# Kernel optimization log

Measured on AMD Instinct MI355X. Metric: run time of the kernel, lower is better.

Reference implementation:

```python
import jax, jax.numpy as jnp
import numpy as np

B, O, T, D, H, DOUT = 32, 4096, 16384, 128, 128, 128
EPS = 1e-3  # keras BatchNormalization default epsilon


def setup_inputs() -> dict:
    key = jax.random.key(0)
    ks = jax.random.split(key, 8)
    std = 0.05  # keras RandomNormal default stddev
    return {
        "obj_vecs": jax.random.normal(ks[0], (B, O, D), jnp.float32),
        "pred_vecs": jax.random.normal(ks[1], (B, T, D), jnp.float32),
        "edges": jax.random.randint(ks[2], (B, T, 2), 0, O, dtype=jnp.int32),
        # net1: [3D -> H] -> BN -> ReLU -> [H -> 2H+Dout] -> BN -> ReLU
        "W1": jax.random.normal(ks[3], (3 * D, H), jnp.float32) * std,
        "b1": jnp.zeros((H,), jnp.float32),
        "g1": jnp.ones((H,), jnp.float32),
        "be1": jnp.zeros((H,), jnp.float32),
        "W2": jax.random.normal(ks[4], (H, 2 * H + DOUT), jnp.float32) * std,
        "b2": jnp.zeros((2 * H + DOUT,), jnp.float32),
        "g2": jnp.ones((2 * H + DOUT,), jnp.float32),
        "be2": jnp.zeros((2 * H + DOUT,), jnp.float32),
        # net2: [H -> H] -> BN -> ReLU -> [H -> Dout] -> BN -> ReLU
        "W3": jax.random.normal(ks[5], (H, H), jnp.float32) * std,
        "b3": jnp.zeros((H,), jnp.float32),
        "g3": jnp.ones((H,), jnp.float32),
        "be3": jnp.zeros((H,), jnp.float32),
        "W4": jax.random.normal(ks[6], (H, DOUT), jnp.float32) * std,
        "b4": jnp.zeros((DOUT,), jnp.float32),
        "g4": jnp.ones((DOUT,), jnp.float32),
        "be4": jnp.zeros((DOUT,), jnp.float32),
    }


def _block(x, W, b, g, be):
    # Dense -> BatchNorm(inference: mean=0, var=1) -> ReLU
    h = x @ W + b
    h = h * (g / jnp.sqrt(1.0 + EPS)) + be
    return jax.nn.relu(h)


def reference(obj_vecs, pred_vecs, edges,
              W1, b1, g1, be1, W2, b2, g2, be2,
              W3, b3, g3, be3, W4, b4, g4, be4):
    s_idx = edges[..., 0]  # (B, T)
    o_idx = edges[..., 1]  # (B, T)

    # gather subject / object vectors: (B, T, D)
    cur_s = jnp.take_along_axis(obj_vecs, s_idx[..., None], axis=1)
    cur_o = jnp.take_along_axis(obj_vecs, o_idx[..., None], axis=1)
    cur_t = jnp.concatenate([cur_s, pred_vecs, cur_o], axis=2)  # (B, T, 3D)

    new_t = _block(_block(cur_t, W1, b1, g1, be1), W2, b2, g2, be2)  # (B, T, 2H+Dout)
    new_s = new_t[..., :H]
    new_p = new_t[..., H:H + DOUT]
    new_o = new_t[..., H + DOUT:]

    # NOTE: original TF code overwrites the s-scatter with the o-scatter,
    # so only object-side messages contribute. scatter_nd sums duplicates.
    bidx = jnp.arange(B)[:, None]  # (B, 1), broadcasts over T
    pooled = jnp.zeros((B, O, H), new_t.dtype).at[bidx, o_idx].add(new_o)
    counts = jnp.zeros((B, O), new_t.dtype).at[bidx, o_idx].add(1.0)
    pooled = pooled / jnp.clip(counts, 1.0, None)[..., None]  # avg pooling

    new_obj = _block(_block(pooled, W3, b3, g3, be3), W4, b4, g4, be4)  # (B, O, Dout)
    return new_obj, new_p
```

## Files before the change

kernel.cpp:

```cpp
#include <hip/hip_runtime.h>
#include <hip/hip_bf16.h>
#include <stdint.h>

#define Bn 32
#define On 4096
#define Tn 16384
#define Dn 128

typedef short short8 __attribute__((ext_vector_type(8)));
typedef float f32x4 __attribute__((ext_vector_type(4)));

__device__ inline short f2bf(float f) {
  union { float f; uint32_t u; } v; v.f = f;
  uint32_t u = v.u;
  uint32_t r = u + 0x7fffu + ((u >> 16) & 1u);
  return (short)(r >> 16);
}
__device__ inline float bf2f(unsigned short u) {
  union { uint32_t ui; float f; } cv; cv.ui = ((uint32_t)u) << 16; return cv.f;
}

__global__ void prep_weights(const float* __restrict__ W1, const float* __restrict__ W2,
                             const float* __restrict__ W3, const float* __restrict__ W4,
                             short* __restrict__ w1t, short* __restrict__ w2t,
                             short* __restrict__ w3t, short* __restrict__ w4t) {
  int i = blockIdx.x * 256 + threadIdx.x;
  if (i < 49152) {
    int n = i / 384, k = i % 384;
    w1t[i] = f2bf(W1[k * 128 + n]);
  } else if (i < 49152 + 32768) {
    int j = i - 49152;
    int n = j / 128, k = j % 128;
    w2t[j] = f2bf(W2[k * 384 + 128 + n]);
  } else if (i < 49152 + 32768 + 16384) {
    int j = i - 81920;
    int n = j / 128, k = j % 128;
    w3t[j] = f2bf(W3[k * 128 + n]);
  } else if (i < 114688) {
    int j = i - 98304;
    int n = j / 128, k = j % 128;
    w4t[j] = f2bf(W4[k * 128 + n]);
  }
}

__global__ __launch_bounds__(1024) void sort_kernel(
    const int* __restrict__ edges, int* __restrict__ hist_g,
    int* __restrict__ offs_g, unsigned short* __restrict__ eidx)
{
  __shared__ int h[4096];
  __shared__ int of[4096];
  __shared__ int sd[1024];
  int b = blockIdx.x, tid = threadIdx.x;
#pragma unroll
  for (int i = 0; i < 4; i++) h[tid + i * 1024] = 0;
  __syncthreads();
  int ov[16];
#pragma unroll
  for (int j = 0; j < 16; j++) {
    int t = j * 1024 + tid;
    ov[j] = edges[((size_t)(b * Tn + t)) * 2 + 1];
    atomicAdd(&h[ov[j]], 1);
  }
  __syncthreads();
  int base = tid * 4;
  int hh[4]; int s = 0;
#pragma unroll
  for (int j = 0; j < 4; j++) { hh[j] = h[base + j]; s += hh[j]; }
  sd[tid] = s;
  int tsum = s;
  for (int off = 1; off < 1024; off <<= 1) {
    __syncthreads();
    int t = (tid >= off) ? sd[tid - off] : 0;
    __syncthreads();
    sd[tid] += t;
  }
  __syncthreads();
  int excl = sd[tid] - tsum + b * Tn;
#pragma unroll
  for (int j = 0; j < 4; j++) {
    of[base + j] = excl;
    offs_g[b * On + base + j] = excl;
    hist_g[b * On + base + j] = hh[j];
    excl += hh[j];
  }
  __syncthreads();
#pragma unroll
  for (int i = 0; i < 4; i++) h[tid + i * 1024] = 0;
  __syncthreads();
#pragma unroll
  for (int j = 0; j < 16; j++) {
    int t = j * 1024 + tid;
    int pos = of[ov[j]] + atomicAdd(&h[ov[j]], 1);
    eidx[pos] = (unsigned short)t;
  }
}

__global__ __launch_bounds__(512, 2) void objproj(
    const float* __restrict__ obj, const short* __restrict__ w1t,
    unsigned short* __restrict__ objSO)
{
  __shared__ __align__(16) char lds[81920];
  const int WOF = 0, AOF = 65536;
  int tid = threadIdx.x;
  {
    int n = tid >> 2, q = tid & 3;
    int swz = (n & 7) << 4;
    const short* s1 = w1t + n * 384 + q * 32;
    const short* s2 = w1t + n * 384 + 256 + q * 32;
#pragma unroll
    for (int i = 0; i < 4; i++) {
      *(short8*)(lds + WOF + n * 256 + ((q * 64 + i * 16) ^ swz)) = *(const short8*)(s1 + i * 8);
      *(short8*)(lds + WOF + 32768 + n * 256 + ((q * 64 + i * 16) ^ swz)) = *(const short8*)(s2 + i * 8);
    }
  }
  int wave = tid >> 6, lane = tid & 63;
  int l15 = lane & 15, l4 = lane >> 4;
  int mg = wave >> 2, ng = wave & 3;
  int r = tid >> 3, seg = tid & 7;
  int rswz = (r & 7) << 4;

  for (int it = 0; it < 4; it++) {
    int row0 = (blockIdx.x * 4 + it) * 64;
    if (it) __syncthreads();
    {
      const float* src = obj + (size_t)(row0 + r) * Dn + seg * 16;
      float4 v0 = *(const float4*)(src);
      float4 v1 = *(const float4*)(src + 4);
      float4 v2 = *(const float4*)(src + 8);
      float4 v3 = *(const float4*)(src + 12);
      short8 p0, p1;
      p0[0]=f2bf(v0.x); p0[1]=f2bf(v0.y); p0[2]=f2bf(v0.z); p0[3]=f2bf(v0.w);
      p0[4]=f2bf(v1.x); p0[5]=f2bf(v1.y); p0[6]=f2bf(v1.z); p0[7]=f2bf(v1.w);
      p1[0]=f2bf(v2.x); p1[1]=f2bf(v2.y); p1[2]=f2bf(v2.z); p1[3]=f2bf(v2.w);
      p1[4]=f2bf(v3.x); p1[5]=f2bf(v3.y); p1[6]=f2bf(v3.z); p1[7]=f2bf(v3.w);
      *(short8*)(lds + AOF + r * 256 + ((seg * 32) ^ rswz)) = p0;
      *(short8*)(lds + AOF + r * 256 + ((seg * 32 + 16) ^ rswz)) = p1;
    }
    __syncthreads();
#pragma unroll
    for (int half = 0; half < 2; half++) {
      f32x4 acc[2][2] = {};
#pragma unroll
      for (int kk = 0; kk < 4; kk++) {
        short8 a[2], bb[2];
#pragma unroll
        for (int m = 0; m < 2; m++) {
          int row = mg * 32 + m * 16 + l15;
          a[m] = *(short8*)(lds + AOF + row * 256 + ((kk * 64 + 16 * l4) ^ ((row & 7) << 4)));
        }
#pragma unroll
        for (int n = 0; n < 2; n++) {
          int nr = ng * 32 + n * 16 + l15;
          bb[n] = *(short8*)(lds + WOF + half * 32768 + nr * 256 + ((kk * 64 + 16 * l4) ^ ((nr & 7) << 4)));
        }
#pragma unroll
        for (int m = 0; m < 2; m++)
#pragma unroll
          for (int n = 0; n < 2; n++)
            acc[m][n] = __builtin_amdgcn_mfma_f32_16x16x32_bf16(a[m], bb[n], acc[m][n], 0, 0, 0);
      }
#pragma unroll
      for (int n = 0; n < 2; n++) {
        int col = ng * 32 + n * 16 + l15;
#pragma unroll
        for (int m = 0; m < 2; m++)
#pragma unroll
          for (int rr = 0; rr < 4; rr++) {
            int row = mg * 32 + m * 16 + l4 * 4 + rr;
            objSO[(size_t)(row0 + row) * 256 + half * 128 + col] =
                (unsigned short)f2bf(acc[m][n][rr]);
          }
      }
    }
  }
}

#define ENT 32
__global__ __launch_bounds__(512, 2) void edge_mlp(
    const float* __restrict__ pred, const int* __restrict__ edges,
    const unsigned short* __restrict__ objSO,
    const short* __restrict__ w1t, const short* __restrict__ w2t,
    const float* __restrict__ b1, const float* __restrict__ g1, const float* __restrict__ be1,
    const float* __restrict__ b2, const float* __restrict__ g2, const float* __restrict__ be2,
    float* __restrict__ out_p, unsigned short* __restrict__ o_scr)
{
  __shared__ __align__(16) char lds[147456];
  const int W1P = 0;
  const int W2O = 32768;
  const int AB0 = 98304;
  const int AB1 = 114688;
  const int GOF = 131072;

  const float invs = 1.0f / sqrtf(1.001f);
  int tid = threadIdx.x;

  {
    int n = tid >> 2, q = tid & 3;
    int swz = (n & 7) << 4;
    const short* src = w1t + n * 384 + 128 + q * 32;
#pragma unroll
    for (int i = 0; i < 4; i++)
      *(short8*)(lds + W1P + n * 256 + ((q * 64 + i * 16) ^ swz)) = *(const short8*)(src + i * 8);
  }
  {
    int n = tid >> 1, q = tid & 1;
    int swz = (n & 7) << 4;
    const short* src = w2t + n * 128 + q * 64;
#pragma unroll
    for (int i = 0; i < 8; i++)
      *(short8*)(lds + W2O + n * 256 + ((q * 128 + i * 16) ^ swz)) = *(const short8*)(src + i * 8);
  }

  int r = tid >> 3, seg = tid & 7;
  int rswz = (r & 7) << 4;

  float4 pv0, pv1, pv2, pv3;
  short8 sv0, sv1, ov0, ov1;

  auto load_tile = [&](int gt) {
    int b_ = gt >> 8;
    int t = ((gt & 255) << 6) + r;
    const float* src = pred + ((size_t)(b_ * Tn + t)) * Dn + seg * 16;
    pv0 = *(const float4*)(src);
    pv1 = *(const float4*)(src + 4);
    pv2 = *(const float4*)(src + 8);
    pv3 = *(const float4*)(src + 12);
    int2 e = *(const int2*)&edges[((size_t)(b_ * Tn + t)) * 2];
    const unsigned short* srow = objSO + ((size_t)(b_ * On + e.x)) * 256 + seg * 16;
    const unsigned short* orow = objSO + ((size_t)(b_ * On + e.y)) * 256 + 128 + seg * 16;
    sv0 = *(const short8*)(srow);
    sv1 = *(const short8*)(srow + 8);
    ov0 = *(const short8*)(orow);
    ov1 = *(const short8*)(orow + 8);
  };

  auto store_stage = [&](int abuf) {
    short8 p0, p1;
    p0[0]=f2bf(pv0.x); p0[1]=f2bf(pv0.y); p0[2]=f2bf(pv0.z); p0[3]=f2bf(pv0.w);
    p0[4]=f2bf(pv1.x); p0[5]=f2bf(pv1.y); p0[6]=f2bf(pv1.z); p0[7]=f2bf(pv1.w);
    p1[0]=f2bf(pv2.x); p1[1]=f2bf(pv2.y); p1[2]=f2bf(pv2.z); p1[3]=f2bf(pv2.w);
    p1[4]=f2bf(pv3.x); p1[5]=f2bf(pv3.y); p1[6]=f2bf(pv3.z); p1[7]=f2bf(pv3.w);
    *(short8*)(lds + abuf + r * 256 + ((seg * 32) ^ rswz)) = p0;
    *(short8*)(lds + abuf + r * 256 + ((seg * 32 + 16) ^ rswz)) = p1;
    short8 g0, g1v;
#pragma unroll
    for (int j = 0; j < 8; j++) {
      g0[j]  = f2bf(bf2f((unsigned short)sv0[j]) + bf2f((unsigned short)ov0[j]));
      g1v[j] = f2bf(bf2f((unsigned short)sv1[j]) + bf2f((unsigned short)ov1[j]));
    }
    *(short8*)(lds + GOF + r * 256 + ((seg * 32) ^ rswz)) = g0;
    *(short8*)(lds + GOF + r * 256 + ((seg * 32 + 16) ^ rswz)) = g1v;
  };

  int tile0 = blockIdx.x * ENT;
  load_tile(tile0);
  store_stage(AB0);
  load_tile(tile0 + 1);
  __syncthreads();

  int wave = tid >> 6, lane = tid & 63;
  int l15 = lane & 15, l4 = lane >> 4;
  int mg = wave >> 2, ng = wave & 3;
  int cur = 0;

  for (int it = 0; it < ENT; ++it) {
    int gt = tile0 + it;
    int b_ = gt >> 8, t0v = (gt & 255) << 6;
    int abuf = cur ? AB1 : AB0;
    int nbuf = cur ? AB0 : AB1;

    f32x4 acc1[2][2] = {};
#pragma unroll
    for (int kk = 0; kk < 4; kk++) {
      short8 a[2], bb[2];
#pragma unroll
      for (int m = 0; m < 2; m++) {
        int row = mg * 32 + m * 16 + l15;
        a[m] = *(short8*)(lds + abuf + row * 256 + ((kk * 64 + 16 * l4) ^ ((row & 7) << 4)));
      }
#pragma unroll
      for (int n = 0; n < 2; n++) {
        int nr = ng * 32 + n * 16 + l15;
        bb[n] = *(short8*)(lds + W1P + nr * 256 + ((kk * 64 + 16 * l4) ^ ((nr & 7) << 4)));
      }
#pragma unroll
      for (int m = 0; m < 2; m++)
#pragma unroll
        for (int n = 0; n < 2; n++)
          acc1[m][n] = __builtin_amdgcn_mfma_f32_16x16x32_bf16(a[m], bb[n], acc1[m][n], 0, 0, 0);
    }
    __syncthreads();

#pragma unroll
    for (int n = 0; n < 2; n++) {
      int col = ng * 32 + n * 16 + l15;
      float gs = g1[col] * invs;
      float add = b1[col] * gs + be1[col];
#pragma unroll
      for (int m = 0; m < 2; m++)
#pragma unroll
        for (int rr = 0; rr < 4; rr++) {
          int row = mg * 32 + m * 16 + l4 * 4 + rr;
          float gv = bf2f(*(const unsigned short*)(lds + GOF + row * 256 + ((col * 2) ^ ((row & 7) << 4))));
          float v = fmaxf((acc1[m][n][rr] + gv) * gs + add, 0.0f);
          *(short*)(lds + abuf + row * 256 + ((col * 2) ^ ((row & 7) << 4))) = f2bf(v);
        }
    }
    __syncthreads();

    if (it + 1 < ENT) store_stage(nbuf);
    if (it + 2 < ENT) load_tile(tile0 + it + 2);

    f32x4 acc2[2][4] = {};
#pragma unroll
    for (int kk = 0; kk < 4; kk++) {
      short8 a[2], bb[4];
#pragma unroll
      for (int m = 0; m < 2; m++) {
        int row = mg * 32 + m * 16 + l15;
        a[m] = *(short8*)(lds + abuf + row * 256 + ((kk * 64 + 16 * l4) ^ ((row & 7) << 4)));
      }
#pragma unroll
      for (int n = 0; n < 4; n++) {
        int nr = ng * 64 + n * 16 + l15;
        bb[n] = *(short8*)(lds + W2O + nr * 256 + ((kk * 64 + 16 * l4) ^ ((nr & 7) << 4)));
      }
#pragma unroll
      for (int m = 0; m < 2; m++)
#pragma unroll
        for (int n = 0; n < 4; n++)
          acc2[m][n] = __builtin_amdgcn_mfma_f32_16x16x32_bf16(a[m], bb[n], acc2[m][n], 0, 0, 0);
    }
#pragma unroll
    for (int n = 0; n < 4; n++) {
      int colp = ng * 64 + n * 16 + l15;
      int c2 = 128 + colp;
      float gs = g2[c2] * invs;
      float add = b2[c2] * gs + be2[c2];
#pragma unroll
      for (int m = 0; m < 2; m++)
#pragma unroll
        for (int rr = 0; rr < 4; rr++) {
          int row = mg * 32 + m * 16 + l4 * 4 + rr;
          float v = fmaxf(acc2[m][n][rr] * gs + add, 0.0f);
          if (colp < 128) {
            out_p[(size_t)(b_ * Tn + t0v + row) * 128 + colp] = v;
          } else {
            o_scr[(size_t)(b_ * Tn + t0v + row) * 128 + (colp - 128)] =
                (unsigned short)f2bf(v);
          }
        }
    }
    __syncthreads();
    cur ^= 1;
  }
}

__global__ __launch_bounds__(256) void obj_mlp(
    const unsigned short* __restrict__ o_scr, const int* __restrict__ hist,
    const int* __restrict__ offs, const unsigned short* __restrict__ eidx,
    float* __restrict__ out_obj,
    const short* __restrict__ w3t, const short* __restrict__ w4t,
    const float* __restrict__ b3, const float* __restrict__ g3, const float* __restrict__ be3,
    const float* __restrict__ b4, const float* __restrict__ g4, const float* __restrict__ be4)
{
  __shared__ short xs[64][136];
  __shared__ short hs[64][136];
  const float invs = 1.0f / sqrtf(1.001f);
  int row0 = blockIdx.x * 64;
  int tid = threadIdx.x;

  {
    int r = tid >> 2, seg = tid & 3;
    int rg = row0 + r;
    int bb_ = rg >> 12;
    int cnt = hist[rg], start = offs[rg];
    float sum[32];
#pragma unroll
    for (int j = 0; j < 32; j++) sum[j] = 0.f;
    for (int k = 0; k < cnt; k++) {
      int t = eidx[start + k];
      const unsigned short* src = o_scr + ((size_t)(bb_ * Tn + t)) * 128 + seg * 32;
#pragma unroll
      for (int i = 0; i < 4; i++) {
        short8 v = *(const short8*)(src + i * 8);
#pragma unroll
        for (int j = 0; j < 8; j++) sum[i * 8 + j] += bf2f((unsigned short)v[j]);
      }
    }
    float ic = 1.0f / fmaxf((float)cnt, 1.0f);
#pragma unroll
    for (int i = 0; i < 4; i++) {
      short8 pk;
#pragma unroll
      for (int j = 0; j < 8; j++) pk[j] = f2bf(sum[i * 8 + j] * ic);
      *(short8*)&xs[r][seg * 32 + i * 8] = pk;
    }
  }
  __syncthreads();

  int wave = tid >> 6, lane = tid & 63;
  int l15 = lane & 15, l4 = lane >> 4;
  int n0 = wave * 32;

  f32x4 acc[4][2] = {};
  for (int kk = 0; kk < 4; kk++) {
    int k0 = kk * 32;
    short8 a[4], bb[2];
#pragma unroll
    for (int m = 0; m < 4; m++) a[m] = *(short8*)&xs[m * 16 + l15][k0 + 8 * l4];
#pragma unroll
    for (int n = 0; n < 2; n++) bb[n] = *(const short8*)&w3t[(n0 + n * 16 + l15) * 128 + k0 + 8 * l4];
#pragma unroll
    for (int m = 0; m < 4; m++)
#pragma unroll
      for (int n = 0; n < 2; n++)
        acc[m][n] = __builtin_amdgcn_mfma_f32_16x16x32_bf16(a[m], bb[n], acc[m][n], 0, 0, 0);
  }
#pragma unroll
  for (int n = 0; n < 2; n++) {
    int col = n0 + n * 16 + l15;
    float gs = g3[col] * invs;
    float add = b3[col] * gs + be3[col];
#pragma unroll
    for (int m = 0; m < 4; m++)
#pragma unroll
      for (int rr = 0; rr < 4; rr++) {
        float v = fmaxf(acc[m][n][rr] * gs + add, 0.0f);
        hs[m * 16 + l4 * 4 + rr][col] = f2bf(v);
      }
  }
  __syncthreads();

  f32x4 acc2[4][2] = {};
  for (int kk = 0; kk < 4; kk++) {
    int k0 = kk * 32;
    short8 a[4], bb[2];
#pragma unroll
    for (int m = 0; m < 4; m++) a[m] = *(short8*)&hs[m * 16 + l15][k0 + 8 * l4];
#pragma unroll
    for (int n = 0; n < 2; n++) bb[n] = *(const short8*)&w4t[(n0 + n * 16 + l15) * 128 + k0 + 8 * l4];
#pragma unroll
    for (int m = 0; m < 4; m++)
#pragma unroll
      for (int n = 0; n < 2; n++)
        acc2[m][n] = __builtin_amdgcn_mfma_f32_16x16x32_bf16(a[m], bb[n], acc2[m][n], 0, 0, 0);
  }
#pragma unroll
  for (int n = 0; n < 2; n++) {
    int col = n0 + n * 16 + l15;
    float gs = g4[col] * invs;
    float add = b4[col] * gs + be4[col];
#pragma unroll
    for (int m = 0; m < 4; m++)
#pragma unroll
      for (int rr = 0; rr < 4; rr++) {
        int row = m * 16 + l4 * 4 + rr;
        float v = fmaxf(acc2[m][n][rr] * gs + add, 0.0f);
        out_obj[(size_t)(row0 + row) * 128 + col] = v;
      }
  }
}

extern "C" void kernel_launch(void* const* d_in, const int* in_sizes, int n_in,
                              void* d_out, int out_size, void* d_ws, size_t ws_size,
                              hipStream_t stream) {
  const float* obj  = (const float*)d_in[0];
  const float* pred = (const float*)d_in[1];
  const int*   edges= (const int*)d_in[2];
  const float* W1 = (const float*)d_in[3];
  const float* b1 = (const float*)d_in[4];
  const float* g1 = (const float*)d_in[5];
  const float* be1= (const float*)d_in[6];
  const float* W2 = (const float*)d_in[7];
  const float* b2 = (const float*)d_in[8];
  const float* g2 = (const float*)d_in[9];
  const float* be2= (const float*)d_in[10];
  const float* W3 = (const float*)d_in[11];
  const float* b3 = (const float*)d_in[12];
  const float* g3 = (const float*)d_in[13];
  const float* be3= (const float*)d_in[14];
  const float* W4 = (const float*)d_in[15];
  const float* b4 = (const float*)d_in[16];
  const float* g4 = (const float*)d_in[17];
  const float* be4= (const float*)d_in[18];

  float* out_obj = (float*)d_out;
  float* out_p   = (float*)d_out + (size_t)Bn * On * 128;
  unsigned short* objSO = (unsigned short*)d_out;

  char* ws = (char*)d_ws;
  short* w1t = (short*)(ws);
  short* w2t = (short*)(ws + 49152 * 2);
  short* w3t = (short*)(ws + (49152 + 32768) * 2);
  short* w4t = (short*)(ws + (49152 + 32768 + 16384) * 2);

  const size_t OFF_HIST = 262144;
  const size_t OFF_OFFS = OFF_HIST + 524288;
  const size_t OFF_EIDX = OFF_OFFS + 1048576;
  const size_t OFF_OSCR = 4194304;

  int* hist = (int*)(ws + OFF_HIST);
  int* offs = (int*)(ws + OFF_OFFS);
  unsigned short* eidx = (unsigned short*)(ws + OFF_EIDX);
  unsigned short* o_scr = (unsigned short*)(ws + OFF_OSCR);

  prep_weights<<<448, 256, 0, stream>>>(W1, W2, W3, W4, w1t, w2t, w3t, w4t);
  sort_kernel<<<Bn, 1024, 0, stream>>>(edges, hist, offs, eidx);
  objproj<<<512, 512, 0, stream>>>(obj, w1t, objSO);
  edge_mlp<<<256, 512, 0, stream>>>(pred, edges, objSO, w1t, w2t,
      b1, g1, be1, b2, g2, be2, out_p, o_scr);
  obj_mlp<<<(Bn * On) / 64, 256, 0, stream>>>(o_scr, hist, offs, eidx, out_obj,
      w3t, w4t, b3, g3, be3, b4, g4, be4);
}
```

Before: 309.1 us.

## Hold MLP weights in registers, shrink LDS, and raise edge_mlp occupancy

The edge_mlp kernel now keeps its W1 and W2 fragments in per-wave registers instead of staging them in LDS. This cuts LDS use from 144KB to 48KB, replaces the double-buffered A tile with single A and H buffers, and launches 768 blocks strided over tiles with launch_bounds of 6. obj_mlp likewise preloads W3 and W4 fragments into registers instead of loading them from global memory inside the k loop. The aim is more resident blocks per CU and fewer LDS and global weight reads, at the cost of heavy register pressure (w2r alone is 64 VGPRs) and the loss of the double-buffered staging.

```diff
diff --git a/kernel.cpp b/kernel.cpp
--- a/kernel.cpp
+++ b/kernel.cpp
@@ -175,8 +175,9 @@
   }
 }
 
-#define ENT 32
-__global__ __launch_bounds__(512, 2) void edge_mlp(
+#define NT_TOTAL 8192
+#define GRID_E 768
+__global__ __launch_bounds__(512, 6) void edge_mlp(
     const float* __restrict__ pred, const int* __restrict__ edges,
     const unsigned short* __restrict__ objSO,
     const short* __restrict__ w1t, const short* __restrict__ w2t,
@@ -184,32 +185,28 @@
     const float* __restrict__ b2, const float* __restrict__ g2, const float* __restrict__ be2,
     float* __restrict__ out_p, unsigned short* __restrict__ o_scr)
 {
-  __shared__ __align__(16) char lds[147456];
-  const int W1P = 0;
-  const int W2O = 32768;
-  const int AB0 = 98304;
-  const int AB1 = 114688;
-  const int GOF = 131072;
+  __shared__ __align__(16) char lds[49152];
+  const int ABUF = 0;
+  const int HBUF = 16384;
+  const int GOF  = 32768;
 
   const float invs = 1.0f / sqrtf(1.001f);
   int tid = threadIdx.x;
-
-  {
-    int n = tid >> 2, q = tid & 3;
-    int swz = (n & 7) << 4;
-    const short* src = w1t + n * 384 + 128 + q * 32;
-#pragma unroll
-    for (int i = 0; i < 4; i++)
-      *(short8*)(lds + W1P + n * 256 + ((q * 64 + i * 16) ^ swz)) = *(const short8*)(src + i * 8);
-  }
-  {
-    int n = tid >> 1, q = tid & 1;
-    int swz = (n & 7) << 4;
-    const short* src = w2t + n * 128 + q * 64;
-#pragma unroll
-    for (int i = 0; i < 8; i++)
-      *(short8*)(lds + W2O + n * 256 + ((q * 128 + i * 16) ^ swz)) = *(const short8*)(src + i * 8);
-  }
+  int wave = tid >> 6, lane = tid & 63;
+  int l15 = lane & 15, l4 = lane >> 4;
+  int mg = wave >> 2, ng = wave & 3;
+
+  short8 w1r[2][4], w2r[4][4];
+#pragma unroll
+  for (int n = 0; n < 2; n++)
+#pragma unroll
+    for (int kk = 0; kk < 4; kk++)
+      w1r[n][kk] = *(const short8*)&w1t[(ng * 32 + n * 16 + l15) * 384 + 128 + kk * 32 + 8 * l4];
+#pragma unroll
+  for (int n = 0; n < 4; n++)
+#pragma unroll
+    for (int kk = 0; kk < 4; kk++)
+      w2r[n][kk] = *(const short8*)&w2t[(ng * 64 + n * 16 + l15) * 128 + kk * 32 + 8 * l4];
 
   int r = tid >> 3, seg = tid & 7;
   int rswz = (r & 7) << 4;
@@ -234,14 +231,14 @@
     ov1 = *(const short8*)(orow + 8);
   };
 
-  auto store_stage = [&](int abuf) {
+  auto store_stage = [&]() {
     short8 p0, p1;
     p0[0]=f2bf(pv0.x); p0[1]=f2bf(pv0.y); p0[2]=f2bf(pv0.z); p0[3]=f2bf(pv0.w);
     p0[4]=f2bf(pv1.x); p0[5]=f2bf(pv1.y); p0[6]=f2bf(pv1.z); p0[7]=f2bf(pv1.w);
     p1[0]=f2bf(pv2.x); p1[1]=f2bf(pv2.y); p1[2]=f2bf(pv2.z); p1[3]=f2bf(pv2.w);
     p1[4]=f2bf(pv3.x); p1[5]=f2bf(pv3.y); p1[6]=f2bf(pv3.z); p1[7]=f2bf(pv3.w);
-    *(short8*)(lds + abuf + r * 256 + ((seg * 32) ^ rswz)) = p0;
-    *(short8*)(lds + abuf + r * 256 + ((seg * 32 + 16) ^ rswz)) = p1;
+    *(short8*)(lds + ABUF + r * 256 + ((seg * 32) ^ rswz)) = p0;
+    *(short8*)(lds + ABUF + r * 256 + ((seg * 32 + 16) ^ rswz)) = p1;
     short8 g0, g1v;
 #pragma unroll
     for (int j = 0; j < 8; j++) {
@@ -252,45 +249,33 @@
     *(short8*)(lds + GOF + r * 256 + ((seg * 32 + 16) ^ rswz)) = g1v;
   };
 
-  int tile0 = blockIdx.x * ENT;
-  load_tile(tile0);
-  store_stage(AB0);
-  load_tile(tile0 + 1);
-  __syncthreads();
-
-  int wave = tid >> 6, lane = tid & 63;
-  int l15 = lane & 15, l4 = lane >> 4;
-  int mg = wave >> 2, ng = wave & 3;
-  int cur = 0;
-
-  for (int it = 0; it < ENT; ++it) {
-    int gt = tile0 + it;
+  int bid = blockIdx.x;
+  int ntiles = (NT_TOTAL - 1 - bid) / GRID_E + 1;
+
+  load_tile(bid);
+  store_stage();
+  if (ntiles > 1) load_tile(bid + GRID_E);
+  __syncthreads();
+
+  for (int k = 0; k < ntiles; ++k) {
+    int gt = bid + k * GRID_E;
     int b_ = gt >> 8, t0v = (gt & 255) << 6;
-    int abuf = cur ? AB1 : AB0;
-    int nbuf = cur ? AB0 : AB1;
 
     f32x4 acc1[2][2] = {};
 #pragma unroll
     for (int kk = 0; kk < 4; kk++) {
-      short8 a[2], bb[2];
+      short8 a[2];
 #pragma unroll
       for (int m = 0; m < 2; m++) {
         int row = mg * 32 + m * 16 + l15;
-        a[m] = *(short8*)(lds + abuf + row * 256 + ((kk * 64 + 16 * l4) ^ ((row & 7) << 4)));
-      }
-#pragma unroll
-      for (int n = 0; n < 2; n++) {
-        int nr = ng * 32 + n * 16 + l15;
-        bb[n] = *(short8*)(lds + W1P + nr * 256 + ((kk * 64 + 16 * l4) ^ ((nr & 7) << 4)));
+        a[m] = *(short8*)(lds + ABUF + row * 256 + ((kk * 64 + 16 * l4) ^ ((row & 7) << 4)));
       }
 #pragma unroll
       for (int m = 0; m < 2; m++)
 #pragma unroll
         for (int n = 0; n < 2; n++)
-          acc1[m][n] = __builtin_amdgcn_mfma_f32_16x16x32_bf16(a[m], bb[n], acc1[m][n], 0, 0, 0);
-    }
-    __syncthreads();
-
+          acc1[m][n] = __builtin_amdgcn_mfma_f32_16x16x32_bf16(a[m], w1r[n][kk], acc1[m][n], 0, 0, 0);
+    }
 #pragma unroll
     for (int n = 0; n < 2; n++) {
       int col = ng * 32 + n * 16 + l15;
@@ -303,33 +288,28 @@
           int row = mg * 32 + m * 16 + l4 * 4 + rr;
           float gv = bf2f(*(const unsigned short*)(lds + GOF + row * 256 + ((col * 2) ^ ((row & 7) << 4))));
           float v = fmaxf((acc1[m][n][rr] + gv) * gs + add, 0.0f);
-          *(short*)(lds + abuf + row * 256 + ((col * 2) ^ ((row & 7) << 4))) = f2bf(v);
+          *(short*)(lds + HBUF + row * 256 + ((col * 2) ^ ((row & 7) << 4))) = f2bf(v);
         }
     }
     __syncthreads();
 
-    if (it + 1 < ENT) store_stage(nbuf);
-    if (it + 2 < ENT) load_tile(tile0 + it + 2);
+    if (k + 1 < ntiles) store_stage();
+    if (k + 2 < ntiles) load_tile(bid + (k + 2) * GRID_E);
 
     f32x4 acc2[2][4] = {};
 #pragma unroll
     for (int kk = 0; kk < 4; kk++) {
-      short8 a[2], bb[4];
+      short8 a[2];
 #pragma unroll
       for (int m = 0; m < 2; m++) {
         int row = mg * 32 + m * 16 + l15;
-        a[m] = *(short8*)(lds + abuf + row * 256 + ((kk * 64 + 16 * l4) ^ ((row & 7) << 4)));
-      }
-#pragma unroll
-      for (int n = 0; n < 4; n++) {
-        int nr = ng * 64 + n * 16 + l15;
-        bb[n] = *(short8*)(lds + W2O + nr * 256 + ((kk * 64 + 16 * l4) ^ ((nr & 7) << 4)));
+        a[m] = *(short8*)(lds + HBUF + row * 256 + ((kk * 64 + 16 * l4) ^ ((row & 7) << 4)));
       }
 #pragma unroll
       for (int m = 0; m < 2; m++)
 #pragma unroll
         for (int n = 0; n < 4; n++)
-          acc2[m][n] = __builtin_amdgcn_mfma_f32_16x16x32_bf16(a[m], bb[n], acc2[m][n], 0, 0, 0);
+          acc2[m][n] = __builtin_amdgcn_mfma_f32_16x16x32_bf16(a[m], w2r[n][kk], acc2[m][n], 0, 0, 0);
     }
 #pragma unroll
     for (int n = 0; n < 4; n++) {
@@ -352,7 +332,6 @@
         }
     }
     __syncthreads();
-    cur ^= 1;
   }
 }
 
@@ -403,19 +382,27 @@
   int l15 = lane & 15, l4 = lane >> 4;
   int n0 = wave * 32;
 
+  short8 w3r[2][4], w4r[2][4];
+#pragma unroll
+  for (int n = 0; n < 2; n++)
+#pragma unroll
+    for (int kk = 0; kk < 4; kk++) {
+      w3r[n][kk] = *(const short8*)&w3t[(n0 + n * 16 + l15) * 128 + kk * 32 + 8 * l4];
+      w4r[n][kk] = *(const short8*)&w4t[(n0 + n * 16 + l15) * 128 + kk * 32 + 8 * l4];
+    }
+
   f32x4 acc[4][2] = {};
+#pragma unroll
   for (int kk = 0; kk < 4; kk++) {
     int k0 = kk * 32;
-    short8 a[4], bb[2];
+    short8 a[4];
 #pragma unroll
     for (int m = 0; m < 4; m++) a[m] = *(short8*)&xs[m * 16 + l15][k0 + 8 * l4];
 #pragma unroll
-    for (int n = 0; n < 2; n++) bb[n] = *(const short8*)&w3t[(n0 + n * 16 + l15) * 128 + k0 + 8 * l4];
-#pragma unroll
     for (int m = 0; m < 4; m++)
 #pragma unroll
       for (int n = 0; n < 2; n++)
-        acc[m][n] = __builtin_amdgcn_mfma_f32_16x16x32_bf16(a[m], bb[n], acc[m][n], 0, 0, 0);
+        acc[m][n] = __builtin_amdgcn_mfma_f32_16x16x32_bf16(a[m], w3r[n][kk], acc[m][n], 0, 0, 0);
   }
 #pragma unroll
   for (int n = 0; n < 2; n++) {
@@ -433,18 +420,17 @@
   __syncthreads();
 
   f32x4 acc2[4][2] = {};
+#pragma unroll
   for (int kk = 0; kk < 4; kk++) {
     int k0 = kk * 32;
-    short8 a[4], bb[2];
+    short8 a[4];
 #pragma unroll
     for (int m = 0; m < 4; m++) a[m] = *(short8*)&hs[m * 16 + l15][k0 + 8 * l4];
 #pragma unroll
-    for (int n = 0; n < 2; n++) bb[n] = *(const short8*)&w4t[(n0 + n * 16 + l15) * 128 + k0 + 8 * l4];
-#pragma unroll
     for (int m = 0; m < 4; m++)
 #pragma unroll
       for (int n = 0; n < 2; n++)
-        acc2[m][n] = __builtin_amdgcn_mfma_f32_16x16x32_bf16(a[m], bb[n], acc2[m][n], 0, 0, 0);
+        acc2[m][n] = __builtin_amdgcn_mfma_f32_16x16x32_bf16(a[m], w4r[n][kk], acc2[m][n], 0, 0, 0);
   }
 #pragma unroll
   for (int n = 0; n < 2; n++) {
@@ -508,7 +494,7 @@
   prep_weights<<<448, 256, 0, stream>>>(W1, W2, W3, W4, w1t, w2t, w3t, w4t);
   sort_kernel<<<Bn, 1024, 0, stream>>>(edges, hist, offs, eidx);
   objproj<<<512, 512, 0, stream>>>(obj, w1t, objSO);
-  edge_mlp<<<256, 512, 0, stream>>>(pred, edges, objSO, w1t, w2t,
+  edge_mlp<<<GRID_E, 512, 0, stream>>>(pred, edges, objSO, w1t, w2t,
       b1, g1, be1, b2, g2, be2, out_p, o_scr);
   obj_mlp<<<(Bn * On) / 64, 256, 0, stream>>>(o_scr, hist, offs, eidx, out_obj,
       w3t, w4t, b3, g3, be3, b4, g4, be4);
```

After: 900.4 us. 191% more time.

## Process edges in object-sorted order and pre-reduce runs inside edge MLP

Applied to the files above, without the earlier changes.

The sort kernel now writes the edges in object-sorted order, packing the subject and pred indices together with a separate sorted object-index array. The edge MLP walks tiles in that order and gathers pred rows through the stored index. It keeps the object-side outputs in LDS and sums each run of equal object indices within a 64-edge tile into one bf16 partial row. obj_mlp then reads only one partial per tile segment instead of one row per edge, and keeps the W3/W4 fragments in registers. The cost is scattered out_p writes and pred reads, an extra serial reduction pass over 128 threads, and more barriers.

```diff
diff --git a/kernel.cpp b/kernel.cpp
--- a/kernel.cpp
+++ b/kernel.cpp
@@ -19,6 +19,12 @@
 __device__ inline float bf2f(unsigned short u) {
   union { uint32_t ui; float f; } cv; cv.ui = ((uint32_t)u) << 16; return cv.f;
 }
+
+#define LBAR() do { \
+  asm volatile("s_waitcnt lgkmcnt(0)" ::: "memory"); \
+  __builtin_amdgcn_sched_barrier(0); \
+  __builtin_amdgcn_s_barrier(); \
+} while (0)
 
 __global__ void prep_weights(const float* __restrict__ W1, const float* __restrict__ W2,
                              const float* __restrict__ W3, const float* __restrict__ W4,
@@ -44,8 +50,9 @@
 }
 
 __global__ __launch_bounds__(1024) void sort_kernel(
-    const int* __restrict__ edges, int* __restrict__ hist_g,
-    int* __restrict__ offs_g, unsigned short* __restrict__ eidx)
+    const int* __restrict__ edges, unsigned short* __restrict__ hist_g,
+    int* __restrict__ offs_g, uint32_t* __restrict__ es4,
+    unsigned short* __restrict__ osort)
 {
   __shared__ int h[4096];
   __shared__ int of[4096];
@@ -54,11 +61,12 @@
 #pragma unroll
   for (int i = 0; i < 4; i++) h[tid + i * 1024] = 0;
   __syncthreads();
-  int ov[16];
+  int ov[16], sv[16];
 #pragma unroll
   for (int j = 0; j < 16; j++) {
     int t = j * 1024 + tid;
-    ov[j] = edges[((size_t)(b * Tn + t)) * 2 + 1];
+    int2 e = *(const int2*)&edges[((size_t)(b * Tn + t)) * 2];
+    sv[j] = e.x; ov[j] = e.y;
     atomicAdd(&h[ov[j]], 1);
   }
   __syncthreads();
@@ -80,7 +88,7 @@
   for (int j = 0; j < 4; j++) {
     of[base + j] = excl;
     offs_g[b * On + base + j] = excl;
-    hist_g[b * On + base + j] = hh[j];
+    hist_g[b * On + base + j] = (unsigned short)hh[j];
     excl += hh[j];
   }
   __syncthreads();
@@ -91,7 +99,8 @@
   for (int j = 0; j < 16; j++) {
     int t = j * 1024 + tid;
     int pos = of[ov[j]] + atomicAdd(&h[ov[j]], 1);
-    eidx[pos] = (unsigned short)t;
+    es4[pos] = (uint32_t)t | ((uint32_t)sv[j] << 16);
+    osort[pos] = (unsigned short)ov[j];
   }
 }
 
@@ -177,14 +186,17 @@
 
 #define ENT 32
 __global__ __launch_bounds__(512, 2) void edge_mlp(
-    const float* __restrict__ pred, const int* __restrict__ edges,
+    const float* __restrict__ pred,
+    const uint32_t* __restrict__ es4, const unsigned short* __restrict__ osort,
     const unsigned short* __restrict__ objSO,
     const short* __restrict__ w1t, const short* __restrict__ w2t,
     const float* __restrict__ b1, const float* __restrict__ g1, const float* __restrict__ be1,
     const float* __restrict__ b2, const float* __restrict__ g2, const float* __restrict__ be2,
-    float* __restrict__ out_p, unsigned short* __restrict__ o_scr)
+    float* __restrict__ out_p, unsigned short* __restrict__ partial)
 {
   __shared__ __align__(16) char lds[147456];
+  __shared__ int trowL[2][64];
+  __shared__ unsigned short osL[2][64];
   const int W1P = 0;
   const int W2O = 32768;
   const int AB0 = 98304;
@@ -214,34 +226,38 @@
   int r = tid >> 3, seg = tid & 7;
   int rswz = (r & 7) << 4;
 
+  uint32_t c_ts; int c_o;
   float4 pv0, pv1, pv2, pv3;
   short8 sv0, sv1, ov0, ov1;
 
   auto load_tile = [&](int gt) {
     int b_ = gt >> 8;
-    int t = ((gt & 255) << 6) + r;
-    const float* src = pred + ((size_t)(b_ * Tn + t)) * Dn + seg * 16;
+    int p0 = gt << 6;
+    c_ts = es4[p0 + r];
+    c_o  = osort[p0 + r];
+    int t = c_ts & 0xFFFF, s = (int)(c_ts >> 16);
+    const float* src = pred + ((size_t)b_ * Tn + t) * Dn + seg * 16;
     pv0 = *(const float4*)(src);
     pv1 = *(const float4*)(src + 4);
     pv2 = *(const float4*)(src + 8);
     pv3 = *(const float4*)(src + 12);
-    int2 e = *(const int2*)&edges[((size_t)(b_ * Tn + t)) * 2];
-    const unsigned short* srow = objSO + ((size_t)(b_ * On + e.x)) * 256 + seg * 16;
-    const unsigned short* orow = objSO + ((size_t)(b_ * On + e.y)) * 256 + 128 + seg * 16;
+    const unsigned short* srow = objSO + ((size_t)b_ * On + s) * 256 + seg * 16;
+    const unsigned short* orow = objSO + ((size_t)b_ * On + c_o) * 256 + 128 + seg * 16;
     sv0 = *(const short8*)(srow);
     sv1 = *(const short8*)(srow + 8);
     ov0 = *(const short8*)(orow);
     ov1 = *(const short8*)(orow + 8);
   };
 
-  auto store_stage = [&](int abuf) {
+  auto store_stage = [&](int slot) {
+    char* ab = lds + (slot ? AB1 : AB0);
     short8 p0, p1;
     p0[0]=f2bf(pv0.x); p0[1]=f2bf(pv0.y); p0[2]=f2bf(pv0.z); p0[3]=f2bf(pv0.w);
     p0[4]=f2bf(pv1.x); p0[5]=f2bf(pv1.y); p0[6]=f2bf(pv1.z); p0[7]=f2bf(pv1.w);
     p1[0]=f2bf(pv2.x); p1[1]=f2bf(pv2.y); p1[2]=f2bf(pv2.z); p1[3]=f2bf(pv2.w);
     p1[4]=f2bf(pv3.x); p1[5]=f2bf(pv3.y); p1[6]=f2bf(pv3.z); p1[7]=f2bf(pv3.w);
-    *(short8*)(lds + abuf + r * 256 + ((seg * 32) ^ rswz)) = p0;
-    *(short8*)(lds + abuf + r * 256 + ((seg * 32 + 16) ^ rswz)) = p1;
+    *(short8*)(ab + r * 256 + ((seg * 32) ^ rswz)) = p0;
+    *(short8*)(ab + r * 256 + ((seg * 32 + 16) ^ rswz)) = p1;
     short8 g0, g1v;
 #pragma unroll
     for (int j = 0; j < 8; j++) {
@@ -250,24 +266,39 @@
     }
     *(short8*)(lds + GOF + r * 256 + ((seg * 32) ^ rswz)) = g0;
     *(short8*)(lds + GOF + r * 256 + ((seg * 32 + 16) ^ rswz)) = g1v;
+    if (seg == 0) { trowL[slot][r] = (int)(c_ts & 0xFFFF); osL[slot][r] = (unsigned short)c_o; }
+  };
+
+  auto reduce_tile = [&](int pb, int p0p) {
+    if (tid < 128) {
+      const char* nb = lds + (pb ? AB1 : AB0);
+      int col = tid;
+      float sum = 0.f; int runstart = 0;
+      for (int i = 0; i < 64; i++) {
+        sum += bf2f(*(const unsigned short*)(nb + i * 256 + ((col * 2) ^ ((i & 7) << 4))));
+        if (i == 63 || osL[pb][i + 1] != osL[pb][i]) {
+          partial[((size_t)(p0p + runstart)) * 128 + col] = (unsigned short)f2bf(sum);
+          sum = 0.f; runstart = i + 1;
+        }
+      }
+    }
   };
 
   int tile0 = blockIdx.x * ENT;
   load_tile(tile0);
-  store_stage(AB0);
+  store_stage(0);
   load_tile(tile0 + 1);
-  __syncthreads();
+  LBAR();
 
   int wave = tid >> 6, lane = tid & 63;
   int l15 = lane & 15, l4 = lane >> 4;
   int mg = wave >> 2, ng = wave & 3;
   int cur = 0;
 
-  for (int it = 0; it < ENT; ++it) {
-    int gt = tile0 + it;
-    int b_ = gt >> 8, t0v = (gt & 255) << 6;
-    int abuf = cur ? AB1 : AB0;
-    int nbuf = cur ? AB0 : AB1;
+  for (int k = 0; k < ENT; ++k) {
+    int gt = tile0 + k;
+    int b_ = gt >> 8;
+    char* Ac = lds + (cur ? AB1 : AB0);
 
     f32x4 acc1[2][2] = {};
 #pragma unroll
@@ -276,7 +307,7 @@
 #pragma unroll
       for (int m = 0; m < 2; m++) {
         int row = mg * 32 + m * 16 + l15;
-        a[m] = *(short8*)(lds + abuf + row * 256 + ((kk * 64 + 16 * l4) ^ ((row & 7) << 4)));
+        a[m] = *(short8*)(Ac + row * 256 + ((kk * 64 + 16 * l4) ^ ((row & 7) << 4)));
       }
 #pragma unroll
       for (int n = 0; n < 2; n++) {
@@ -289,7 +320,8 @@
         for (int n = 0; n < 2; n++)
           acc1[m][n] = __builtin_amdgcn_mfma_f32_16x16x32_bf16(a[m], bb[n], acc1[m][n], 0, 0, 0);
     }
-    __syncthreads();
+    if (k > 0) reduce_tile((k - 1) & 1, (gt - 1) << 6);
+    LBAR();
 
 #pragma unroll
     for (int n = 0; n < 2; n++) {
@@ -303,13 +335,13 @@
           int row = mg * 32 + m * 16 + l4 * 4 + rr;
           float gv = bf2f(*(const unsigned short*)(lds + GOF + row * 256 + ((col * 2) ^ ((row & 7) << 4))));
           float v = fmaxf((acc1[m][n][rr] + gv) * gs + add, 0.0f);
-          *(short*)(lds + abuf + row * 256 + ((col * 2) ^ ((row & 7) << 4))) = f2bf(v);
+          *(short*)(Ac + row * 256 + ((col * 2) ^ ((row & 7) << 4))) = f2bf(v);
         }
     }
-    __syncthreads();
-
-    if (it + 1 < ENT) store_stage(nbuf);
-    if (it + 2 < ENT) load_tile(tile0 + it + 2);
+    LBAR();
+
+    if (k + 1 < ENT) store_stage((k + 1) & 1);
+    if (k + 2 < ENT) load_tile(tile0 + k + 2);
 
     f32x4 acc2[2][4] = {};
 #pragma unroll
@@ -318,7 +350,7 @@
 #pragma unroll
       for (int m = 0; m < 2; m++) {
         int row = mg * 32 + m * 16 + l15;
-        a[m] = *(short8*)(lds + abuf + row * 256 + ((kk * 64 + 16 * l4) ^ ((row & 7) << 4)));
+        a[m] = *(short8*)(Ac + row * 256 + ((kk * 64 + 16 * l4) ^ ((row & 7) << 4)));
       }
 #pragma unroll
       for (int n = 0; n < 4; n++) {
@@ -331,6 +363,8 @@
         for (int n = 0; n < 4; n++)
           acc2[m][n] = __builtin_amdgcn_mfma_f32_16x16x32_bf16(a[m], bb[n], acc2[m][n], 0, 0, 0);
     }
+    LBAR();
+
 #pragma unroll
     for (int n = 0; n < 4; n++) {
       int colp = ng * 64 + n * 16 + l15;
@@ -344,22 +378,21 @@
           int row = mg * 32 + m * 16 + l4 * 4 + rr;
           float v = fmaxf(acc2[m][n][rr] * gs + add, 0.0f);
           if (colp < 128) {
-            out_p[(size_t)(b_ * Tn + t0v + row) * 128 + colp] = v;
+            out_p[((size_t)b_ * Tn + trowL[cur][row]) * 128 + colp] = v;
           } else {
-            o_scr[(size_t)(b_ * Tn + t0v + row) * 128 + (colp - 128)] =
-                (unsigned short)f2bf(v);
+            *(short*)(Ac + row * 256 + (((colp - 128) * 2) ^ ((row & 7) << 4))) = f2bf(v);
           }
         }
     }
-    __syncthreads();
+    LBAR();
     cur ^= 1;
   }
+  reduce_tile((ENT - 1) & 1, (tile0 + ENT - 1) << 6);
 }
 
 __global__ __launch_bounds__(256) void obj_mlp(
-    const unsigned short* __restrict__ o_scr, const int* __restrict__ hist,
-    const int* __restrict__ offs, const unsigned short* __restrict__ eidx,
-    float* __restrict__ out_obj,
+    const unsigned short* __restrict__ partial, const unsigned short* __restrict__ hist,
+    const int* __restrict__ offs, float* __restrict__ out_obj,
     const short* __restrict__ w3t, const short* __restrict__ w4t,
     const float* __restrict__ b3, const float* __restrict__ g3, const float* __restrict__ be3,
     const float* __restrict__ b4, const float* __restrict__ g4, const float* __restrict__ be4)
@@ -373,20 +406,21 @@
   {
     int r = tid >> 2, seg = tid & 3;
     int rg = row0 + r;
-    int bb_ = rg >> 12;
-    int cnt = hist[rg], start = offs[rg];
+    int cnt = (int)hist[rg];
+    int start = offs[rg];
     float sum[32];
 #pragma unroll
     for (int j = 0; j < 32; j++) sum[j] = 0.f;
-    for (int k = 0; k < cnt; k++) {
-      int t = eidx[start + k];
-      const unsigned short* src = o_scr + ((size_t)(bb_ * Tn + t)) * 128 + seg * 32;
+    int p = start, pend = start + cnt;
+    while (p < pend) {
+      const unsigned short* src = partial + (size_t)p * 128 + seg * 32;
 #pragma unroll
       for (int i = 0; i < 4; i++) {
         short8 v = *(const short8*)(src + i * 8);
 #pragma unroll
         for (int j = 0; j < 8; j++) sum[i * 8 + j] += bf2f((unsigned short)v[j]);
       }
+      p = ((p >> 6) + 1) << 6;
     }
     float ic = 1.0f / fmaxf((float)cnt, 1.0f);
 #pragma unroll
@@ -403,19 +437,27 @@
   int l15 = lane & 15, l4 = lane >> 4;
   int n0 = wave * 32;
 
+  short8 w3r[2][4], w4r[2][4];
+#pragma unroll
+  for (int n = 0; n < 2; n++)
+#pragma unroll
+    for (int kk = 0; kk < 4; kk++) {
+      w3r[n][kk] = *(const short8*)&w3t[(n0 + n * 16 + l15) * 128 + kk * 32 + 8 * l4];
+      w4r[n][kk] = *(const short8*)&w4t[(n0 + n * 16 + l15) * 128 + kk * 32 + 8 * l4];
+    }
+
   f32x4 acc[4][2] = {};
+#pragma unroll
   for (int kk = 0; kk < 4; kk++) {
     int k0 = kk * 32;
-    short8 a[4], bb[2];
+    short8 a[4];
 #pragma unroll
     for (int m = 0; m < 4; m++) a[m] = *(short8*)&xs[m * 16 + l15][k0 + 8 * l4];
 #pragma unroll
-    for (int n = 0; n < 2; n++) bb[n] = *(const short8*)&w3t[(n0 + n * 16 + l15) * 128 + k0 + 8 * l4];
-#pragma unroll
     for (int m = 0; m < 4; m++)
 #pragma unroll
       for (int n = 0; n < 2; n++)
-        acc[m][n] = __builtin_amdgcn_mfma_f32_16x16x32_bf16(a[m], bb[n], acc[m][n], 0, 0, 0);
+        acc[m][n] = __builtin_amdgcn_mfma_f32_16x16x32_bf16(a[m], w3r[n][kk], acc[m][n], 0, 0, 0);
   }
 #pragma unroll
   for (int n = 0; n < 2; n++) {
@@ -433,18 +475,17 @@
   __syncthreads();
 
   f32x4 acc2[4][2] = {};
+#pragma unroll
   for (int kk = 0; kk < 4; kk++) {
     int k0 = kk * 32;
-    short8 a[4], bb[2];
+    short8 a[4];
 #pragma unroll
     for (int m = 0; m < 4; m++) a[m] = *(short8*)&hs[m * 16 + l15][k0 + 8 * l4];
 #pragma unroll
-    for (int n = 0; n < 2; n++) bb[n] = *(const short8*)&w4t[(n0 + n * 16 + l15) * 128 + k0 + 8 * l4];
-#pragma unroll
     for (int m = 0; m < 4; m++)
 #pragma unroll
       for (int n = 0; n < 2; n++)
-        acc2[m][n] = __builtin_amdgcn_mfma_f32_16x16x32_bf16(a[m], bb[n], acc2[m][n], 0, 0, 0);
+        acc2[m][n] = __builtin_amdgcn_mfma_f32_16x16x32_bf16(a[m], w4r[n][kk], acc2[m][n], 0, 0, 0);
   }
 #pragma unroll
   for (int n = 0; n < 2; n++) {
@@ -494,22 +535,17 @@
   short* w2t = (short*)(ws + 49152 * 2);
   short* w3t = (short*)(ws + (49152 + 32768) * 2);
   short* w4t = (short*)(ws + (49152 + 32768 + 16384) * 2);
-
-  const size_t OFF_HIST = 262144;
-  const size_t OFF_OFFS = OFF_HIST + 524288;
-  const size_t OFF_EIDX = OFF_OFFS + 1048576;
-  const size_t OFF_OSCR = 4194304;
-
-  int* hist = (int*)(ws + OFF_HIST);
-  int* offs = (int*)(ws + OFF_OFFS);
-  unsigned short* eidx = (unsigned short*)(ws + OFF_EIDX);
-  unsigned short* o_scr = (unsigned short*)(ws + OFF_OSCR);
+  unsigned short* hist = (unsigned short*)(ws + 262144);
+  int* offs = (int*)(ws + 524288);
+  uint32_t* es4 = (uint32_t*)(ws + 1048576);
+  unsigned short* osort = (unsigned short*)(ws + 3145728);
+  unsigned short* partial = (unsigned short*)(ws + 4194304);
 
   prep_weights<<<448, 256, 0, stream>>>(W1, W2, W3, W4, w1t, w2t, w3t, w4t);
-  sort_kernel<<<Bn, 1024, 0, stream>>>(edges, hist, offs, eidx);
+  sort_kernel<<<Bn, 1024, 0, stream>>>(edges, hist, offs, es4, osort);
   objproj<<<512, 512, 0, stream>>>(obj, w1t, objSO);
-  edge_mlp<<<256, 512, 0, stream>>>(pred, edges, objSO, w1t, w2t,
-      b1, g1, be1, b2, g2, be2, out_p, o_scr);
-  obj_mlp<<<(Bn * On) / 64, 256, 0, stream>>>(o_scr, hist, offs, eidx, out_obj,
+  edge_mlp<<<256, 512, 0, stream>>>(pred, es4, osort, objSO, w1t, w2t,
+      b1, g1, be1, b2, g2, be2, out_p, partial);
+  obj_mlp<<<(Bn * On) / 64, 256, 0, stream>>>(partial, hist, offs, out_obj,
       w3t, w4t, b3, g3, be3, b4, g4, be4);
 }
```

Result: slower. 484.3 us (+56.6%).

## Split edge MLP LDS buffers, cut barriers, and preload obj MLP weights into registers

Applied to the files above, without the earlier changes.

In edge_mlp, the double-buffered A tiles become a single input buffer plus a separate hidden buffer, so the first-layer output goes to HBUF instead of overwriting the input. This lets the loop drop one of its three barriers per iteration, and the remaining ones become a custom LDS-only barrier that waits only on lgkmcnt, not on outstanding global loads. In obj_mlp, the W3/W4 B fragments are loaded into registers before the GEMM loops instead of being reloaded inside them. The risks are LDS races if the reduced synchronisation is insufficient (for example, store_stage for the next tile overwriting ABUF while the GOF tile is still being read) and higher register pressure in obj_mlp.

```diff
diff --git a/kernel.cpp b/kernel.cpp
--- a/kernel.cpp
+++ b/kernel.cpp
@@ -19,6 +19,12 @@
 __device__ inline float bf2f(unsigned short u) {
   union { uint32_t ui; float f; } cv; cv.ui = ((uint32_t)u) << 16; return cv.f;
 }
+
+#define LBAR() do { \
+  asm volatile("s_waitcnt lgkmcnt(0)" ::: "memory"); \
+  __builtin_amdgcn_sched_barrier(0); \
+  __builtin_amdgcn_s_barrier(); \
+} while (0)
 
 __global__ void prep_weights(const float* __restrict__ W1, const float* __restrict__ W2,
                              const float* __restrict__ W3, const float* __restrict__ W4,
@@ -187,8 +193,8 @@
   __shared__ __align__(16) char lds[147456];
   const int W1P = 0;
   const int W2O = 32768;
-  const int AB0 = 98304;
-  const int AB1 = 114688;
+  const int ABUF = 98304;
+  const int HBUF = 114688;
   const int GOF = 131072;
 
   const float invs = 1.0f / sqrtf(1.001f);
@@ -234,14 +240,14 @@
     ov1 = *(const short8*)(orow + 8);
   };
 
-  auto store_stage = [&](int abuf) {
+  auto store_stage = [&]() {
     short8 p0, p1;
     p0[0]=f2bf(pv0.x); p0[1]=f2bf(pv0.y); p0[2]=f2bf(pv0.z); p0[3]=f2bf(pv0.w);
     p0[4]=f2bf(pv1.x); p0[5]=f2bf(pv1.y); p0[6]=f2bf(pv1.z); p0[7]=f2bf(pv1.w);
     p1[0]=f2bf(pv2.x); p1[1]=f2bf(pv2.y); p1[2]=f2bf(pv2.z); p1[3]=f2bf(pv2.w);
     p1[4]=f2bf(pv3.x); p1[5]=f2bf(pv3.y); p1[6]=f2bf(pv3.z); p1[7]=f2bf(pv3.w);
-    *(short8*)(lds + abuf + r * 256 + ((seg * 32) ^ rswz)) = p0;
-    *(short8*)(lds + abuf + r * 256 + ((seg * 32 + 16) ^ rswz)) = p1;
+    *(short8*)(lds + ABUF + r * 256 + ((seg * 32) ^ rswz)) = p0;
+    *(short8*)(lds + ABUF + r * 256 + ((seg * 32 + 16) ^ rswz)) = p1;
     short8 g0, g1v;
 #pragma unroll
     for (int j = 0; j < 8; j++) {
@@ -253,21 +259,18 @@
   };
 
   int tile0 = blockIdx.x * ENT;
-  load_tile(tile0);
-  store_stage(AB0);
-  load_tile(tile0 + 1);
-  __syncthreads();
-
   int wave = tid >> 6, lane = tid & 63;
   int l15 = lane & 15, l4 = lane >> 4;
   int mg = wave >> 2, ng = wave & 3;
-  int cur = 0;
-
-  for (int it = 0; it < ENT; ++it) {
-    int gt = tile0 + it;
+
+  load_tile(tile0);
+  store_stage();
+  load_tile(tile0 + 1);
+  LBAR();
+
+  for (int k = 0; k < ENT; ++k) {
+    int gt = tile0 + k;
     int b_ = gt >> 8, t0v = (gt & 255) << 6;
-    int abuf = cur ? AB1 : AB0;
-    int nbuf = cur ? AB0 : AB1;
 
     f32x4 acc1[2][2] = {};
 #pragma unroll
@@ -276,7 +279,7 @@
 #pragma unroll
       for (int m = 0; m < 2; m++) {
         int row = mg * 32 + m * 16 + l15;
-        a[m] = *(short8*)(lds + abuf + row * 256 + ((kk * 64 + 16 * l4) ^ ((row & 7) << 4)));
+        a[m] = *(short8*)(lds + ABUF + row * 256 + ((kk * 64 + 16 * l4) ^ ((row & 7) << 4)));
       }
 #pragma unroll
       for (int n = 0; n < 2; n++) {
@@ -289,8 +292,6 @@
         for (int n = 0; n < 2; n++)
           acc1[m][n] = __builtin_amdgcn_mfma_f32_16x16x32_bf16(a[m], bb[n], acc1[m][n], 0, 0, 0);
     }
-    __syncthreads();
-
 #pragma unroll
     for (int n = 0; n < 2; n++) {
       int col = ng * 32 + n * 16 + l15;
@@ -303,13 +304,13 @@
           int row = mg * 32 + m * 16 + l4 * 4 + rr;
           float gv = bf2f(*(const unsigned short*)(lds + GOF + row * 256 + ((col * 2) ^ ((row & 7) << 4))));
           float v = fmaxf((acc1[m][n][rr] + gv) * gs + add, 0.0f);
-          *(short*)(lds + abuf + row * 256 + ((col * 2) ^ ((row & 7) << 4))) = f2bf(v);
+          *(short*)(lds + HBUF + row * 256 + ((col * 2) ^ ((row & 7) << 4))) = f2bf(v);
         }
     }
-    __syncthreads();
-
-    if (it + 1 < ENT) store_stage(nbuf);
-    if (it + 2 < ENT) load_tile(tile0 + it + 2);
+    LBAR();
+
+    if (k + 1 < ENT) store_stage();
+    if (k + 2 < ENT) load_tile(tile0 + k + 2);
 
     f32x4 acc2[2][4] = {};
 #pragma unroll
@@ -318,7 +319,7 @@
 #pragma unroll
       for (int m = 0; m < 2; m++) {
         int row = mg * 32 + m * 16 + l15;
-        a[m] = *(short8*)(lds + abuf + row * 256 + ((kk * 64 + 16 * l4) ^ ((row & 7) << 4)));
+        a[m] = *(short8*)(lds + HBUF + row * 256 + ((kk * 64 + 16 * l4) ^ ((row & 7) << 4)));
       }
 #pragma unroll
       for (int n = 0; n < 4; n++) {
@@ -351,8 +352,7 @@
           }
         }
     }
-    __syncthreads();
-    cur ^= 1;
+    LBAR();
   }
 }
 
@@ -403,19 +403,27 @@
   int l15 = lane & 15, l4 = lane >> 4;
   int n0 = wave * 32;
 
+  short8 w3r[2][4], w4r[2][4];
+#pragma unroll
+  for (int n = 0; n < 2; n++)
+#pragma unroll
+    for (int kk = 0; kk < 4; kk++) {
+      w3r[n][kk] = *(const short8*)&w3t[(n0 + n * 16 + l15) * 128 + kk * 32 + 8 * l4];
+      w4r[n][kk] = *(const short8*)&w4t[(n0 + n * 16 + l15) * 128 + kk * 32 + 8 * l4];
+    }
+
   f32x4 acc[4][2] = {};
+#pragma unroll
   for (int kk = 0; kk < 4; kk++) {
     int k0 = kk * 32;
-    short8 a[4], bb[2];
+    short8 a[4];
 #pragma unroll
     for (int m = 0; m < 4; m++) a[m] = *(short8*)&xs[m * 16 + l15][k0 + 8 * l4];
 #pragma unroll
-    for (int n = 0; n < 2; n++) bb[n] = *(const short8*)&w3t[(n0 + n * 16 + l15) * 128 + k0 + 8 * l4];
-#pragma unroll
     for (int m = 0; m < 4; m++)
 #pragma unroll
       for (int n = 0; n < 2; n++)
-        acc[m][n] = __builtin_amdgcn_mfma_f32_16x16x32_bf16(a[m], bb[n], acc[m][n], 0, 0, 0);
+        acc[m][n] = __builtin_amdgcn_mfma_f32_16x16x32_bf16(a[m], w3r[n][kk], acc[m][n], 0, 0, 0);
   }
 #pragma unroll
   for (int n = 0; n < 2; n++) {
@@ -433,18 +441,17 @@
   __syncthreads();
 
   f32x4 acc2[4][2] = {};
+#pragma unroll
   for (int kk = 0; kk < 4; kk++) {
     int k0 = kk * 32;
-    short8 a[4], bb[2];
+    short8 a[4];
 #pragma unroll
     for (int m = 0; m < 4; m++) a[m] = *(short8*)&hs[m * 16 + l15][k0 + 8 * l4];
 #pragma unroll
-    for (int n = 0; n < 2; n++) bb[n] = *(const short8*)&w4t[(n0 + n * 16 + l15) * 128 + k0 + 8 * l4];
-#pragma unroll
     for (int m = 0; m < 4; m++)
 #pragma unroll
       for (int n = 0; n < 2; n++)
-        acc2[m][n] = __builtin_amdgcn_mfma_f32_16x16x32_bf16(a[m], bb[n], acc2[m][n], 0, 0, 0);
+        acc2[m][n] = __builtin_amdgcn_mfma_f32_16x16x32_bf16(a[m], w4r[n][kk], acc2[m][n], 0, 0, 0);
   }
 #pragma unroll
   for (int n = 0; n < 2; n++) {
```

New measurement: 324.4 us. +4.9%, slower.
